# Kernel optimization log

Hardware: AMD Instinct MI355X
Metric: run time of the kernel (lower is better)

## Reference

```python
import jax, jax.numpy as jnp
import numpy as np

B, N, NPOINT, K = 8, 4096, 512, 32
D_IN, D_POS, D_OUT = 64, 64, 128
D = D_IN + D_POS  # 128, channel dim entering Double_SA
EPS = 1e-5


def _gather(pts, idx):
    # pts [B,N,C], idx [B,...] -> [B,...,C]
    return jax.vmap(lambda p, i: p[i])(pts, idx)


def _bn(x, p):
    # eval-mode BatchNorm over last (channel) dim; p = [gamma, beta, mean, var]
    g, b, m, v = p
    return g * (x - m) * jax.lax.rsqrt(v + EPS) + b


def _fps(xyz, start):
    # iterative farthest point sampling, vectorized over batch
    Bb, Nn, _ = xyz.shape
    def step(carry, _):
        dist, far = carry  # dist [B,N], far [B]
        c = jnp.take_along_axis(xyz, far[:, None, None], axis=1)  # [B,1,3]
        d = jnp.sum((xyz - c) ** 2, -1)
        dist = jnp.minimum(dist, d)
        return (dist, jnp.argmax(dist, -1)), far
    init = (jnp.full((Bb, Nn), 1e10, xyz.dtype), start)
    _, idx = jax.lax.scan(step, init, None, length=NPOINT)
    return idx.T  # [B, NPOINT]


def _forward(xyz, points, fps_start, pos_w1, pos_b1, pos_bn1, pos_w2, pos_b2, pos_bn2,
             nsa_wq, nsa_bq, nsa_wk, nsa_bk, nsa_wv, nsa_bv, nsa_gamma, gam_gamma,
             cat_w1, cat_b1, cat_bn1, cat_w2, cat_b2, cat_bn2, sc_w, sc_b, sc_bn):
    fps_idx = _fps(xyz, fps_start)                 # [B,S]
    center_xyz = _gather(xyz, fps_idx)             # [B,S,3]
    # brute-force KNN: squared distances center -> all points, take k smallest
    d2 = (jnp.sum(center_xyz ** 2, -1)[:, :, None] + jnp.sum(xyz ** 2, -1)[:, None, :]
          - 2.0 * jnp.einsum('bsc,bnc->bsn', center_xyz, xyz))  # [B,S,N]
    neg_d, knn_idx = jax.lax.top_k(-d2, K)
    knn_dist = -neg_d                               # [B,S,K], ascending
    grouped_xyz = _gather(xyz, knn_idx)             # [B,S,K,3]
    grouped_pts = _gather(points, knn_idx)          # [B,S,K,D_IN]
    # PosEmbeding: cat(center, neighbor, relative, dist) -> MLP(10 -> Dpos/2 -> Dpos)
    center = jnp.broadcast_to(center_xyz[:, :, None, :], grouped_xyz.shape)
    feat = jnp.concatenate([center, grouped_xyz, grouped_xyz - center, knn_dist[..., None]], -1)
    h = jax.nn.relu(_bn(feat @ pos_w1 + pos_b1, pos_bn1))
    pos = jax.nn.relu(_bn(h @ pos_w2 + pos_b2, pos_bn2))
    x = jnp.concatenate([pos, grouped_pts], -1)     # [B,S,K,D]
    # Neighbor_SA_New: per-group self-attention over K neighbors
    q = x @ nsa_wq + nsa_bq                         # [B,S,K,D//8]
    k = x @ nsa_wk + nsa_bk
    v = x @ nsa_wv + nsa_bv                         # [B,S,K,D]
    attn = jax.nn.softmax(jnp.einsum('bskc,bsjc->bskj', q, k), axis=-1)
    nei = nsa_gamma * jnp.einsum('bskj,bsjd->bskd', attn, v) + x
    # GAM: attention between groups over flattened K*D features
    flat = x.reshape(B, NPOINT, K * D)
    ga = jax.nn.softmax(jnp.einsum('bsd,btd->bst', flat, flat), axis=-1)  # [B,S,S]
    grp = gam_gamma * jnp.einsum('bst,btd->bsd', ga, flat).reshape(B, NPOINT, K, D) + x
    dsa = jnp.concatenate([nei, grp], -1)           # [B,S,K,2D]
    main = _bn(jax.nn.relu(_bn(dsa @ cat_w1 + cat_b1, cat_bn1)) @ cat_w2 + cat_b2, cat_bn2)
    sc = jax.nn.relu(_bn(grouped_pts @ sc_w + sc_b, sc_bn))
    new_points = jnp.max(jax.nn.relu(main + sc), axis=2)  # [B,S,D_OUT]
    return center_xyz, new_points


def setup_inputs():
    ks = jax.random.split(jax.random.key(0), 40)
    def w(i, shape, s=0.05):
        return s * jax.random.normal(ks[i], shape, jnp.float32)
    def bnp(i, c):
        k1, k2, k3, k4 = jax.random.split(ks[i], 4)
        return jnp.stack([jax.random.uniform(k1, (c,), jnp.float32, 0.5, 1.5),
                          0.1 * jax.random.normal(k2, (c,), jnp.float32),
                          0.1 * jax.random.normal(k3, (c,), jnp.float32),
                          jax.random.uniform(k4, (c,), jnp.float32, 0.5, 1.5)])
    return dict(
        xyz=jax.random.normal(ks[0], (B, N, 3), jnp.float32),
        points=jax.random.normal(ks[1], (B, N, D_IN), jnp.float32),
        fps_start=jax.random.randint(ks[2], (B,), 0, N),
        pos_w1=w(3, (10, D_POS // 2)), pos_b1=w(4, (D_POS // 2,)), pos_bn1=bnp(5, D_POS // 2),
        pos_w2=w(6, (D_POS // 2, D_POS)), pos_b2=w(7, (D_POS,)), pos_bn2=bnp(8, D_POS),
        nsa_wq=w(9, (D, D // 8)), nsa_bq=w(10, (D // 8,)),
        nsa_wk=w(11, (D, D // 8)), nsa_bk=w(12, (D // 8,)),
        nsa_wv=w(13, (D, D)), nsa_bv=w(14, (D,)),
        nsa_gamma=jnp.array([0.5], jnp.float32),
        gam_gamma=jnp.array([0.5], jnp.float32),
        cat_w1=w(15, (2 * D, 2 * D)), cat_b1=w(16, (2 * D,)), cat_bn1=bnp(17, 2 * D),
        cat_w2=w(18, (2 * D, D_OUT)), cat_b2=w(19, (D_OUT,)), cat_bn2=bnp(20, D_OUT),
        sc_w=w(21, (D_IN, D_OUT)), sc_b=w(22, (D_OUT,)), sc_bn=bnp(23, D_OUT),
    )


def reference(xyz, points, fps_start, pos_w1, pos_b1, pos_bn1, pos_w2, pos_b2, pos_bn2,
              nsa_wq, nsa_bq, nsa_wk, nsa_bk, nsa_wv, nsa_bv, nsa_gamma, gam_gamma,
              cat_w1, cat_b1, cat_bn1, cat_w2, cat_b2, cat_bn2, sc_w, sc_b, sc_bn):
    return _forward(xyz, points, fps_start, pos_w1, pos_b1, pos_bn1, pos_w2, pos_b2, pos_bn2,
                    nsa_wq, nsa_bq, nsa_wk, nsa_bk, nsa_wv, nsa_bv, nsa_gamma, gam_gamma,
                    cat_w1, cat_b1, cat_bn1, cat_w2, cat_b2, cat_bn2, sc_w, sc_b, sc_bn)
```

## Files before the change

### kernel.cpp

```cpp
#include <hip/hip_runtime.h>
#include <stdint.h>
#include <float.h>

typedef unsigned int uint;

#define NB 8
#define NPTS 4096
#define NS 512
#define NKN 32

__device__ int   g_fps_idx[NB*NS];
__device__ int   g_knn_idx[NB*NS*NKN];
__device__ float g_knn_d2 [NB*NS*NKN];
__device__ float g_posb   [(size_t)NB*NS*NKN*64];
__device__ float g_ga     [(size_t)NB*NS*NS];
__device__ float g_gp     [(size_t)4*NB*NS*NS];
__device__ float g_dsa    [(size_t)NB*NS*NKN*256];

__device__ __forceinline__ unsigned long long shfl_down_u64(unsigned long long v, int off){
  int lo = __shfl_down((int)(unsigned)v, off);
  int hi = __shfl_down((int)(unsigned)(v >> 32), off);
  return ((unsigned long long)(unsigned)hi << 32) | (unsigned)lo;
}
__device__ __forceinline__ unsigned long long u64max(unsigned long long a, unsigned long long b){
  return a > b ? a : b;
}
__device__ __forceinline__ unsigned long long u64min(unsigned long long a, unsigned long long b){
  return a < b ? a : b;
}
__device__ __forceinline__ void ldf8(const float* p, float* d){
  float4 a = *(const float4*)p, b = *(const float4*)(p+4);
  d[0]=a.x; d[1]=a.y; d[2]=a.z; d[3]=a.w; d[4]=b.x; d[5]=b.y; d[6]=b.z; d[7]=b.w;
}
__device__ __forceinline__ int read_start(const int* __restrict__ start, int b){
  int w1 = start[1], w3 = start[3], w5 = start[5], w7 = start[7];
  bool is64 = ((w1 | w3 | w5 | w7) == 0);
  int v = is64 ? start[2*b] : start[b];
  return v & (NPTS - 1);
}

__device__ __forceinline__ void load_flat8(const float* __restrict__ points,
                                           int b, int row, int n, float* d){
  const int k = n >> 7, col = n & 63;
  if (n & 64){
    const int idx = g_knn_idx[((b << 9) + row)*32 + k];
    ldf8(points + (((size_t)b << 12) + idx)*64 + col, d);
  } else {
    ldf8(g_posb + (((size_t)((b << 9) + row))*32 + k)*64 + col, d);
  }
}
__device__ __forceinline__ float4 load_flat4(const float* __restrict__ points,
                                             int b, int row, int n){
  const int k = n >> 7, d = n & 127;
  if (d & 64){
    const int idx = g_knn_idx[((b << 9) + row)*32 + k];
    return *(const float4*)(points + (((size_t)b << 12) + idx)*64 + (d & 63));
  } else {
    return *(const float4*)(g_posb + (((size_t)((b << 9) + row))*32 + k)*64 + d);
  }
}
__device__ __forceinline__ void load_gram8(const float* __restrict__ points,
                                           int b, int row, int kc, float* d){
  if (kc < 2048){
    ldf8(g_posb + ((size_t)((b << 9) + row))*2048 + kc, d);
  } else {
    const int kc2 = kc - 2048, kg = kc2 >> 6, col = kc2 & 63;
    const int idx = g_knn_idx[((b << 9) + row)*32 + kg];
    ldf8(points + (((size_t)b << 12) + idx)*64 + col, d);
  }
}

__global__ __launch_bounds__(256) void k_fps(const float* __restrict__ xyz,
                                             const int* __restrict__ start,
                                             float* __restrict__ center_out){
#pragma clang fp contract(off)
  const int b = blockIdx.x, tid = threadIdx.x;
  const float* X = xyz + (size_t)b * NPTS * 3;
  __shared__ float sx[NPTS], sy[NPTS], sz[NPTS];
  for (int p = tid; p < NPTS; p += 256){
    sx[p] = X[3*p]; sy[p] = X[3*p+1]; sz[p] = X[3*p+2];
  }
  __shared__ int s_start0;
  if (tid == 0) s_start0 = read_start(start, b);
  __syncthreads();
  float px[16], py[16], pz[16], dist[16];
  for (int i = 0; i < 16; i++){
    int p = tid*16 + i;
    px[i] = sx[p]; py[i] = sy[p]; pz[i] = sz[p];
    dist[i] = 1e10f;
  }
  __shared__ unsigned long long s_k[2][4];
  int cur = s_start0;
  for (int t = 0; t < NS; t++){
    if (tid == 0){
      g_fps_idx[b*NS + t] = cur;
      center_out[(size_t)(b*NS + t)*3 + 0] = sx[cur];
      center_out[(size_t)(b*NS + t)*3 + 1] = sy[cur];
      center_out[(size_t)(b*NS + t)*3 + 2] = sz[cur];
    }
    const float cx = sx[cur], cy = sy[cur], cz = sz[cur];
    float bv = -1.0f; int bi = 0;
#pragma unroll
    for (int i = 0; i < 16; i++){
      float dx = px[i]-cx, dy = py[i]-cy, dz = pz[i]-cz;
      float d = ((dx*dx) + (dy*dy)) + (dz*dz);
      dist[i] = fminf(dist[i], d);
      if (dist[i] > bv){ bv = dist[i]; bi = i; }
    }
    unsigned long long bk = ((unsigned long long)__float_as_uint(bv) << 32)
                          | (unsigned)(NPTS-1 - (tid*16 + bi));
    { unsigned long long a = shfl_down_u64(bk,16), c = shfl_down_u64(bk,32), d = shfl_down_u64(bk,48);
      bk = u64max(u64max(bk,a), u64max(c,d)); }
    { unsigned long long a = shfl_down_u64(bk,4),  c = shfl_down_u64(bk,8),  d = shfl_down_u64(bk,12);
      bk = u64max(u64max(bk,a), u64max(c,d)); }
    { unsigned long long a = shfl_down_u64(bk,1),  c = shfl_down_u64(bk,2),  d = shfl_down_u64(bk,3);
      bk = u64max(u64max(bk,a), u64max(c,d)); }
    const int par = t & 1;
    if ((tid & 63) == 0) s_k[par][tid>>6] = bk;
    __syncthreads();
    unsigned long long m = u64max(u64max(s_k[par][0], s_k[par][1]),
                                  u64max(s_k[par][2], s_k[par][3]));
    cur = NPTS-1 - (int)(unsigned)m;
  }
}

__global__ __launch_bounds__(256) void k_knn(const float* __restrict__ xyz){
#pragma clang fp contract(off)
  const int g = blockIdx.x;
  const int b = g >> 9;
  const int tid = threadIdx.x;
  const float* X = xyz + (size_t)b * NPTS * 3;
  const int cidx = g_fps_idx[g];
  const float cx = X[3*cidx], cy = X[3*cidx+1], cz = X[3*cidx+2];
  const float cs = ((cx*cx) + (cy*cy)) + (cz*cz);
  unsigned long long kl[16];
#pragma unroll
  for (int i = 0; i < 16; i++){
    int p = tid*16 + i;
    float x = X[3*p], y = X[3*p+1], z = X[3*p+2];
    float xs2 = ((x*x) + (y*y)) + (z*z);
    float dt  = ((cx*x) + (cy*y)) + (cz*z);
    float d   = (cs + xs2) - 2.0f*dt;
    unsigned bits = __float_as_uint(d);
    unsigned mono = (bits & 0x80000000u) ? ~bits : (bits ^ 0x80000000u);
    kl[i] = ((unsigned long long)mono << 32) | (unsigned)p;
  }
  __shared__ unsigned long long s_w[2][4];
  unsigned long long last = 0;
  for (int sel = 0; sel < NKN; sel++){
    unsigned long long mk[16];
#pragma unroll
    for (int i = 0; i < 16; i++)
      mk[i] = (kl[i] > last) ? kl[i] : 0xFFFFFFFFFFFFFFFFULL;
#pragma unroll
    for (int st = 8; st; st >>= 1)
      for (int i = 0; i < st; i++) mk[i] = u64min(mk[i], mk[i+st]);
    unsigned long long bk = mk[0];
    { unsigned long long a = shfl_down_u64(bk,16), c = shfl_down_u64(bk,32), d = shfl_down_u64(bk,48);
      bk = u64min(u64min(bk,a), u64min(c,d)); }
    { unsigned long long a = shfl_down_u64(bk,4),  c = shfl_down_u64(bk,8),  d = shfl_down_u64(bk,12);
      bk = u64min(u64min(bk,a), u64min(c,d)); }
    { unsigned long long a = shfl_down_u64(bk,1),  c = shfl_down_u64(bk,2),  d = shfl_down_u64(bk,3);
      bk = u64min(u64min(bk,a), u64min(c,d)); }
    const int par = sel & 1;
    if ((tid & 63) == 0) s_w[par][tid>>6] = bk;
    __syncthreads();
    unsigned long long m = u64min(u64min(s_w[par][0], s_w[par][1]),
                                  u64min(s_w[par][2], s_w[par][3]));
    last = m;
    if (tid == 0){
      unsigned hm = (unsigned)(m >> 32);
      unsigned bits = (hm & 0x80000000u) ? (hm ^ 0x80000000u) : ~hm;
      g_knn_idx[g*NKN + sel] = (int)(unsigned)m;
      g_knn_d2 [g*NKN + sel] = __uint_as_float(bits);
    }
  }
}

__global__ __launch_bounds__(256) void k_posembed(
    const float* __restrict__ xyz,
    const float* __restrict__ w1, const float* __restrict__ b1, const float* __restrict__ bn1,
    const float* __restrict__ w2, const float* __restrict__ b2, const float* __restrict__ bn2){
  __shared__ float w1s[320], a1s[32], d1s[32], w2s[2048], a2s[64], d2s[64];
  const int t = threadIdx.x;
  for (int i = t; i < 320; i += 256) w1s[i] = w1[i];
  for (int i = t; i < 2048; i += 256) w2s[i] = w2[i];
  if (t < 32){
    float g = bn1[t], be = bn1[32+t], m = bn1[64+t], v = bn1[96+t];
    float a = g * rsqrtf(v + 1e-5f);
    a1s[t] = a; d1s[t] = b1[t]*a + (be - m*a);
  }
  if (t < 64){
    float g = bn2[t], be = bn2[64+t], m = bn2[128+t], v = bn2[192+t];
    float a = g * rsqrtf(v + 1e-5f);
    a2s[t] = a; d2s[t] = b2[t]*a + (be - m*a);
  }
  __syncthreads();
  const int row = blockIdx.x*256 + t;
  const int b = row >> 14;
  const int g = row >> 5;
  const float* X = xyz + (size_t)b * NPTS * 3;
  const int ci = g_fps_idx[g];
  const int ni = g_knn_idx[row];
  float c0 = X[3*ci], c1 = X[3*ci+1], c2 = X[3*ci+2];
  float n0 = X[3*ni], n1 = X[3*ni+1], n2 = X[3*ni+2];
  float feat[10] = {c0,c1,c2, n0,n1,n2, n0-c0,n1-c1,n2-c2, g_knn_d2[row]};
  float h[32];
  for (int o = 0; o < 32; o++){
    float acc = 0.f;
    for (int j = 0; j < 10; j++) acc += feat[j]*w1s[j*32+o];
    h[o] = fmaxf(acc*a1s[o] + d1s[o], 0.f);
  }
  float* xr = g_posb + (size_t)row * 64;
  for (int o = 0; o < 64; o++){
    float acc = 0.f;
    for (int j = 0; j < 32; j++) acc += h[j]*w2s[j*64+o];
    xr[o] = fmaxf(acc*a2s[o] + d2s[o], 0.f);
  }
}

__global__ __launch_bounds__(256) void k_gram(const float* __restrict__ points){
  const int b = blockIdx.y, ch = blockIdx.z;
  int ti = 0, rem = blockIdx.x;
  while (rem >= 8 - ti){ rem -= 8 - ti; ti++; }
  const int tj = ti + rem;
  const int i0 = ti * 64, j0 = tj * 64;
  __shared__ float As[32][68];
  __shared__ float Bs[32][68];
  const int t = threadIdx.x, tx = t & 15, ty = t >> 4;
  float acc[4][4] = {};
  const int kbeg = ch * 1024, kend = kbeg + 1024;
  for (int k0 = kbeg; k0 < kend; k0 += 32){
    {
      int r = t >> 2, kk = (t & 3) * 8;
      float ta[8], tb[8];
      load_gram8(points, b, i0+r, k0+kk, ta);
      load_gram8(points, b, j0+r, k0+kk, tb);
      for (int jj = 0; jj < 8; jj++){
        int k = kk + jj;
        int c = (r + (k & 24)) & 63;
        As[k][c] = ta[jj]; Bs[k][c] = tb[jj];
      }
    }
    __syncthreads();
    for (int kk = 0; kk < 32; kk++){
      const int rot = kk & 24;
      const float4 a4 = *(const float4*)(&As[kk][(ty*4 + rot) & 63]);
      const float4 b4 = *(const float4*)(&Bs[kk][(tx*4 + rot) & 63]);
      const float ar[4] = {a4.x,a4.y,a4.z,a4.w};
      const float br[4] = {b4.x,b4.y,b4.z,b4.w};
      for (int ia = 0; ia < 4; ia++)
        for (int ib = 0; ib < 4; ib++) acc[ia][ib] += ar[ia]*br[ib];
    }
    __syncthreads();
  }
  float* C = g_gp + ((size_t)(ch*NB + b)) * NS * NS;
  for (int ia = 0; ia < 4; ia++){
    float4 o = {acc[ia][0], acc[ia][1], acc[ia][2], acc[ia][3]};
    *(float4*)(C + (size_t)(i0+ty*4+ia)*NS + j0 + tx*4) = o;
  }
  if (ti != tj){
    for (int ib = 0; ib < 4; ib++){
      float4 o = {acc[0][ib], acc[1][ib], acc[2][ib], acc[3][ib]};
      *(float4*)(C + (size_t)(j0+tx*4+ib)*NS + i0 + ty*4) = o;
    }
  }
}

__global__ __launch_bounds__(256) void k_gsm(){
  const size_t N = (size_t)NB * NS * NS;
  const size_t base = (size_t)blockIdx.x * NS;
  const int t = threadIdx.x;
  float v0, v1;
  {
    float a0 = g_gp[base + t],       b0 = g_gp[N + base + t];
    float c0 = g_gp[2*N + base + t], d0 = g_gp[3*N + base + t];
    v0 = ((a0 + b0) + c0) + d0;
    float a1 = g_gp[base + t + 256],       b1 = g_gp[N + base + t + 256];
    float c1 = g_gp[2*N + base + t + 256], d1 = g_gp[3*N + base + t + 256];
    v1 = ((a1 + b1) + c1) + d1;
  }
  __shared__ float sm[4], ssum[4];
  float m = fmaxf(v0, v1);
  for (int off = 32; off; off >>= 1) m = fmaxf(m, __shfl_down(m, off));
  if ((t & 63) == 0) sm[t>>6] = m;
  __syncthreads();
  float mm = fmaxf(fmaxf(sm[0], sm[1]), fmaxf(sm[2], sm[3]));
  float e0 = expf(v0 - mm), e1 = expf(v1 - mm);
  float s = e0 + e1;
  for (int off = 32; off; off >>= 1) s += __shfl_down(s, off);
  if ((t & 63) == 0) ssum[t>>6] = s;
  __syncthreads();
  float inv = 1.0f / (ssum[0]+ssum[1]+ssum[2]+ssum[3]);
  g_ga[base + t] = e0*inv;
  g_ga[base + t + 256] = e1*inv;
}

__global__ __launch_bounds__(256) void k_grp(const float* __restrict__ points,
                                             const float* __restrict__ gam_g){
  const int b = blockIdx.y;
  const int s0 = (blockIdx.x >> 6) * 64, n0 = (blockIdx.x & 63) * 64;
  const float* G = g_ga + (size_t)b * NS * NS;
  __shared__ float As[32][68];
  __shared__ float Bs[32][68];
  const int t = threadIdx.x, tx = t & 15, ty = t >> 4;
  float acc[4][4] = {};
  for (int k0 = 0; k0 < NS; k0 += 32){
    {
      int r = t >> 2, kk = (t & 3) * 8;
      const float* pa = G + (size_t)(s0+r)*NS + k0 + kk;
      float4 v0 = *(const float4*)pa, v1 = *(const float4*)(pa+4);
      const float va[8] = {v0.x,v0.y,v0.z,v0.w,v1.x,v1.y,v1.z,v1.w};
      for (int jj = 0; jj < 8; jj++){
        int k = kk + jj;
        As[k][(r + (k & 24)) & 63] = va[jj];
      }
      int k2 = t >> 3, c = (t & 7) * 8;
      float tb[8];
      load_flat8(points, b, k0+k2, n0+c, tb);
      float4 w0 = {tb[0],tb[1],tb[2],tb[3]}, w1 = {tb[4],tb[5],tb[6],tb[7]};
      *(float4*)(&Bs[k2][c])   = w0;
      *(float4*)(&Bs[k2][c+4]) = w1;
    }
    __syncthreads();
    for (int kk = 0; kk < 32; kk++){
      const float4 a4 = *(const float4*)(&As[kk][(ty*4 + (kk & 24)) & 63]);
      const float4 b4 = *(const float4*)(&Bs[kk][tx*4]);
      const float ar[4] = {a4.x,a4.y,a4.z,a4.w};
      const float br[4] = {b4.x,b4.y,b4.z,b4.w};
      for (int ia = 0; ia < 4; ia++)
        for (int ib = 0; ib < 4; ib++) acc[ia][ib] += ar[ia]*br[ib];
    }
    __syncthreads();
  }
  const float gmg = gam_g[0];
  const int n = n0 + tx*4;
  const int kq = n >> 7, dq = n & 127;
  for (int ia = 0; ia < 4; ia++){
    int s = s0 + ty*4 + ia;
    float4 xv = load_flat4(points, b, s, n);
    float4 o = {gmg*acc[ia][0]+xv.x, gmg*acc[ia][1]+xv.y,
                gmg*acc[ia][2]+xv.z, gmg*acc[ia][3]+xv.w};
    *(float4*)(g_dsa + ((size_t)((b*NS + s)*32 + kq))*256 + 128 + dq) = o;
  }
}

__global__ __launch_bounds__(256) void k_nsa(const float* __restrict__ points,
    const float* __restrict__ wq, const float* __restrict__ bq,
    const float* __restrict__ wk, const float* __restrict__ bk,
    const float* __restrict__ wv, const float* __restrict__ bv_,
    const float* __restrict__ nsa_g){
  const int g = blockIdx.y*512 + blockIdx.x;
  const int t = threadIdx.x, b = g >> 9;
  const int r = t >> 3, c = t & 7;
  __shared__ float xs[32][132];
  __shared__ float vs[32][132];
  __shared__ float qs[32][17], ks[32][17];
  __shared__ float at[32][33];
  __shared__ float wqs[2048];
  __shared__ float wks[2048];
  __shared__ float wvs[4096];
  {
    float tmp[8];
    ldf8(g_posb + ((size_t)g*32 + r)*64 + c*8, tmp);
    for (int j = 0; j < 8; j++) xs[r][c*8+j] = tmp[j];
    int idx = g_knn_idx[g*32 + r];
    ldf8(points + ((size_t)b*NPTS + idx)*64 + c*8, tmp);
    for (int j = 0; j < 8; j++) xs[r][64+c*8+j] = tmp[j];
  }
  for (int i = t; i < 512; i += 256){
    ((float4*)wqs)[i] = ((const float4*)wq)[i];
    ((float4*)wks)[i] = ((const float4*)wk)[i];
  }
  __syncthreads();
  {
    float aq0 = bq[c], aq1 = bq[c+8], ak0 = bk[c], ak1 = bk[c+8];
#pragma unroll 8
    for (int j = 0; j < 128; j++){
      float xv = xs[r][j];
      aq0 += xv * wqs[j*16+c];
      aq1 += xv * wqs[j*16+c+8];
      ak0 += xv * wks[j*16+c];
      ak1 += xv * wks[j*16+c+8];
    }
    qs[r][c] = aq0; qs[r][c+8] = aq1; ks[r][c] = ak0; ks[r][c+8] = ak1;
  }
  {
    const float4* bv4 = (const float4*)bv_;
    float4 va = bv4[c], vb = bv4[8+c], vc4 = bv4[16+c], vd = bv4[24+c];
#pragma unroll 1
    for (int t4 = 0; t4 < 4; t4++){
      if (t4) __syncthreads();
      for (int i = t; i < 1024; i += 256)
        ((float4*)wvs)[i] = ((const float4*)wv)[(size_t)t4*1024 + i];
      __syncthreads();
#pragma unroll 4
      for (int jl = 0; jl < 32; jl++){
        float xv = xs[r][t4*32 + jl];
        const float4* row = (const float4*)(wvs + jl*128);
        float4 w0 = row[c], w1 = row[8+c], w2 = row[16+c], w3 = row[24+c];
        va.x += xv*w0.x;  va.y += xv*w0.y;  va.z += xv*w0.z;  va.w += xv*w0.w;
        vb.x += xv*w1.x;  vb.y += xv*w1.y;  vb.z += xv*w1.z;  vb.w += xv*w1.w;
        vc4.x += xv*w2.x; vc4.y += xv*w2.y; vc4.z += xv*w2.z; vc4.w += xv*w2.w;
        vd.x += xv*w3.x;  vd.y += xv*w3.y;  vd.z += xv*w3.z;  vd.w += xv*w3.w;
      }
    }
    float4* vrow = (float4*)(&vs[r][0]);
    vrow[c] = va; vrow[8+c] = vb; vrow[16+c] = vc4; vrow[24+c] = vd;
  }
  __syncthreads();
  float p0, p1, p2, p3;
  {
    float s[4];
    for (int jj = 0; jj < 4; jj++){
      int j = 4*c + jj; float acc = 0.f;
      for (int cc = 0; cc < 16; cc++) acc += qs[r][cc] * ks[j][cc];
      s[jj] = acc;
    }
    float m = fmaxf(fmaxf(s[0], s[1]), fmaxf(s[2], s[3]));
    m = fmaxf(m, __shfl_xor(m, 1));
    m = fmaxf(m, __shfl_xor(m, 2));
    m = fmaxf(m, __shfl_xor(m, 4));
    float e0 = expf(s[0]-m), e1 = expf(s[1]-m), e2 = expf(s[2]-m), e3 = expf(s[3]-m);
    float sum = ((e0 + e1) + (e2 + e3));
    sum += __shfl_xor(sum, 1);
    sum += __shfl_xor(sum, 2);
    sum += __shfl_xor(sum, 4);
    float inv = 1.0f / sum;
    p0 = e0*inv; p1 = e1*inv; p2 = e2*inv; p3 = e3*inv;
    at[r][4*c+0] = p0; at[r][4*c+1] = p1; at[r][4*c+2] = p2; at[r][4*c+3] = p3;
  }
  {
    float4 a0 = {0,0,0,0}, a1 = {0,0,0,0}, a2 = {0,0,0,0}, a3 = {0,0,0,0};
    for (int j = 0; j < 32; j++){
      float a = at[r][j];
      const float4* vrow = (const float4*)(&vs[j][0]);
      float4 w0 = vrow[c], w1 = vrow[8+c], w2 = vrow[16+c], w3 = vrow[24+c];
      a0.x += a*w0.x; a0.y += a*w0.y; a0.z += a*w0.z; a0.w += a*w0.w;
      a1.x += a*w1.x; a1.y += a*w1.y; a1.z += a*w1.z; a1.w += a*w1.w;
      a2.x += a*w2.x; a2.y += a*w2.y; a2.z += a*w2.z; a2.w += a*w2.w;
      a3.x += a*w3.x; a3.y += a*w3.y; a3.z += a*w3.z; a3.w += a*w3.w;
    }
    const float gmn = nsa_g[0];
    float* dst = g_dsa + ((size_t)g*32 + r)*256;
    float4 x0 = *(const float4*)(&xs[r][ 0+4*c]);
    float4 x1 = *(const float4*)(&xs[r][32+4*c]);
    float4 x2 = *(const float4*)(&xs[r][64+4*c]);
    float4 x3 = *(const float4*)(&xs[r][96+4*c]);
    float4 o0 = {gmn*a0.x+x0.x, gmn*a0.y+x0.y, gmn*a0.z+x0.z, gmn*a0.w+x0.w};
    float4 o1 = {gmn*a1.x+x1.x, gmn*a1.y+x1.y, gmn*a1.z+x1.z, gmn*a1.w+x1.w};
    float4 o2 = {gmn*a2.x+x2.x, gmn*a2.y+x2.y, gmn*a2.z+x2.z, gmn*a2.w+x2.w};
    float4 o3 = {gmn*a3.x+x3.x, gmn*a3.y+x3.y, gmn*a3.z+x3.z, gmn*a3.w+x3.w};
    *(float4*)(dst +  0 + 4*c) = o0;
    *(float4*)(dst + 32 + 4*c) = o1;
    *(float4*)(dst + 64 + 4*c) = o2;
    *(float4*)(dst + 96 + 4*c) = o3;
  }
}

__global__ __launch_bounds__(256) void k_mlp(const float* __restrict__ points,
    const float* __restrict__ w1, const float* __restrict__ b1, const float* __restrict__ bn1,
    const float* __restrict__ w2, const float* __restrict__ b2, const float* __restrict__ bn2,
    const float* __restrict__ wsc, const float* __restrict__ bsc, const float* __restrict__ bnsc,
    float* __restrict__ out){
  const int g = blockIdx.y*512 + blockIdx.x;
  const int t = threadIdx.x, b = g >> 9;
  __shared__ float ds[32][260];
  __shared__ float hs[32][260];
  __shared__ float ps[32][68];
  __shared__ float a1s[256], d1s[256];
  __shared__ float red[256];
  for (int i = t; i < 2048; i += 256){
    int r = i >> 6, c = (i & 63) * 4;
    *(float4*)(&ds[r][c]) = *(const float4*)(g_dsa + ((size_t)g*32 + r)*256 + c);
  }
  for (int i = t; i < 512; i += 256){
    int r = i >> 4, c = (i & 15) * 4;
    int idx = g_knn_idx[g*32 + r];
    *(float4*)(&ps[r][c]) = *(const float4*)(points + ((size_t)b*NPTS + idx)*64 + c);
  }
  {
    float gg2 = bn1[t], be = bn1[256+t], m = bn1[512+t], v = bn1[768+t];
    float a = gg2 * rsqrtf(v + 1e-5f);
    a1s[t] = a; d1s[t] = b1[t]*a + (be - m*a);
  }
  __syncthreads();
  {
    const int kg = t >> 6, c0 = (t & 63) * 4;
    float acc[8][4] = {};
    for (int j = 0; j < 256; j += 4){
      float wvv[4][4];
      for (int jj = 0; jj < 4; jj++){
        float4 wrow = *(const float4*)(w1 + (j+jj)*256 + c0);
        wvv[jj][0] = wrow.x; wvv[jj][1] = wrow.y; wvv[jj][2] = wrow.z; wvv[jj][3] = wrow.w;
      }
      for (int r = 0; r < 8; r++){
        const float4 d4 = *(const float4*)(&ds[kg*8+r][j]);
        const float dr[4] = {d4.x, d4.y, d4.z, d4.w};
        for (int jj = 0; jj < 4; jj++)
          for (int i = 0; i < 4; i++) acc[r][i] += dr[jj]*wvv[jj][i];
      }
    }
    for (int r = 0; r < 8; r++){
      float4 o;
      o.x = fmaxf(acc[r][0]*a1s[c0+0] + d1s[c0+0], 0.f);
      o.y = fmaxf(acc[r][1]*a1s[c0+1] + d1s[c0+1], 0.f);
      o.z = fmaxf(acc[r][2]*a1s[c0+2] + d1s[c0+2], 0.f);
      o.w = fmaxf(acc[r][3]*a1s[c0+3] + d1s[c0+3], 0.f);
      *(float4*)(&hs[kg*8+r][c0]) = o;
    }
  }
  __syncthreads();
  {
    const int c = t & 127, kh = t >> 7;
    float g2 = bn2[c], be2 = bn2[128+c], m2 = bn2[256+c], v2 = bn2[384+c];
    float a2 = g2 * rsqrtf(v2 + 1e-5f);
    float d2v = b2[c]*a2 + (be2 - m2*a2);
    float gsc = bnsc[c], besc = bnsc[128+c], msc = bnsc[256+c], vsc = bnsc[384+c];
    float asc = gsc * rsqrtf(vsc + 1e-5f);
    float dscv = bsc[c]*asc + (besc - msc*asc);
    float accm[16] = {};
    for (int j = 0; j < 256; j += 4){
      float w0 = w2[j*128+c], w1v = w2[(j+1)*128+c];
      float w2v = w2[(j+2)*128+c], w3 = w2[(j+3)*128+c];
      for (int r = 0; r < 16; r++){
        const float4 h4 = *(const float4*)(&hs[kh*16+r][j]);
        accm[r] += h4.x*w0; accm[r] += h4.y*w1v; accm[r] += h4.z*w2v; accm[r] += h4.w*w3;
      }
    }
    float accs[16] = {};
    for (int j = 0; j < 64; j += 4){
      float w0 = wsc[j*128+c], w1v = wsc[(j+1)*128+c];
      float w2v = wsc[(j+2)*128+c], w3 = wsc[(j+3)*128+c];
      for (int r = 0; r < 16; r++){
        const float4 p4 = *(const float4*)(&ps[kh*16+r][j]);
        accs[r] += p4.x*w0; accs[r] += p4.y*w1v; accs[r] += p4.z*w2v; accs[r] += p4.w*w3;
      }
    }
    float mx = -1e30f;
    for (int r = 0; r < 16; r++){
      float mainv = accm[r]*a2 + d2v;
      float scv = fmaxf(accs[r]*asc + dscv, 0.f);
      mx = fmaxf(mx, fmaxf(mainv + scv, 0.f));
    }
    red[t] = mx;
  }
  __syncthreads();
  if (t < 128){
    float m = fmaxf(red[t], red[t+128]);
    out[12288 + (size_t)g*128 + t] = m;
  }
}

extern "C" void kernel_launch(void* const* d_in, const int* in_sizes, int n_in,
                              void* d_out, int out_size, void* d_ws, size_t ws_size,
                              hipStream_t stream){
  (void)in_sizes; (void)n_in; (void)d_ws; (void)ws_size; (void)out_size;
  const float* xyz      = (const float*)d_in[0];
  const float* points   = (const float*)d_in[1];
  const int*   fstart   = (const int*)  d_in[2];
  const float* pos_w1   = (const float*)d_in[3];
  const float* pos_b1   = (const float*)d_in[4];
  const float* pos_bn1  = (const float*)d_in[5];
  const float* pos_w2   = (const float*)d_in[6];
  const float* pos_b2   = (const float*)d_in[7];
  const float* pos_bn2  = (const float*)d_in[8];
  const float* nsa_wq   = (const float*)d_in[9];
  const float* nsa_bq   = (const float*)d_in[10];
  const float* nsa_wk   = (const float*)d_in[11];
  const float* nsa_bk   = (const float*)d_in[12];
  const float* nsa_wv   = (const float*)d_in[13];
  const float* nsa_bv   = (const float*)d_in[14];
  const float* nsa_g    = (const float*)d_in[15];
  const float* gam_g    = (const float*)d_in[16];
  const float* cat_w1   = (const float*)d_in[17];
  const float* cat_b1   = (const float*)d_in[18];
  const float* cat_bn1  = (const float*)d_in[19];
  const float* cat_w2   = (const float*)d_in[20];
  const float* cat_b2   = (const float*)d_in[21];
  const float* cat_bn2  = (const float*)d_in[22];
  const float* sc_w     = (const float*)d_in[23];
  const float* sc_b     = (const float*)d_in[24];
  const float* sc_bn    = (const float*)d_in[25];
  float* out = (float*)d_out;

  k_fps     <<<NB, 256, 0, stream>>>(xyz, fstart, out);
  k_knn     <<<NB*NS, 256, 0, stream>>>(xyz);
  k_posembed<<<512, 256, 0, stream>>>(xyz, pos_w1, pos_b1, pos_bn1, pos_w2, pos_b2, pos_bn2);
  k_gram    <<<dim3(36, NB, 4), 256, 0, stream>>>(points);
  k_gsm     <<<NB*NS, 256, 0, stream>>>();
  k_grp     <<<dim3(512, NB), 256, 0, stream>>>(points, gam_g);
  k_nsa     <<<dim3(512, NB), 256, 0, stream>>>(points, nsa_wq, nsa_bq, nsa_wk, nsa_bk,
                                                nsa_wv, nsa_bv, nsa_g);
  k_mlp     <<<dim3(512, NB), 256, 0, stream>>>(points, cat_w1, cat_b1, cat_bn1,
                                                cat_w2, cat_b2, cat_bn2,
                                                sc_w, sc_b, sc_bn, out);
}
```

Before: 1.680 ms.

## Fuse position-embedding MLP into KNN kernel and vectorize point loads

Merges the separate position-embedding kernel into the KNN kernel, so the neighbour indices and distances stay in shared memory instead of going through a global buffer and a second launch. The xyz coordinates are now loaded with float4 vector reads, and the per-selection min scan replaces the masked tree reduction with a single conditional loop. Each block now also loads the MLP weights and does the embedding work for its 32 neighbours, split across 8 threads per row with float4 stores. The cost is extra shared memory and register pressure in the KNN kernel, and the weight loads are repeated in all 4096 blocks.

```diff
diff --git a/kernel.cpp b/kernel.cpp
--- a/kernel.cpp
+++ b/kernel.cpp
@@ -11,7 +11,6 @@
 
 __device__ int   g_fps_idx[NB*NS];
 __device__ int   g_knn_idx[NB*NS*NKN];
-__device__ float g_knn_d2 [NB*NS*NKN];
 __device__ float g_posb   [(size_t)NB*NS*NKN*64];
 __device__ float g_ga     [(size_t)NB*NS*NS];
 __device__ float g_gp     [(size_t)4*NB*NS*NS];
@@ -124,20 +123,47 @@
   }
 }
 
-__global__ __launch_bounds__(256) void k_knn(const float* __restrict__ xyz){
+__global__ __launch_bounds__(256) void k_knn(const float* __restrict__ xyz,
+    const float* __restrict__ w1, const float* __restrict__ b1, const float* __restrict__ bn1,
+    const float* __restrict__ w2, const float* __restrict__ b2, const float* __restrict__ bn2){
 #pragma clang fp contract(off)
   const int g = blockIdx.x;
   const int b = g >> 9;
   const int tid = threadIdx.x;
   const float* X = xyz + (size_t)b * NPTS * 3;
+  __shared__ float w1s[320], a1s[32], d1s[32], w2s[2048], a2s[64], d2s[64];
+  __shared__ int   s_ni[32];
+  __shared__ float s_nd[32];
+  __shared__ unsigned long long s_w[2][4];
+  for (int i = tid; i < 320; i += 256) w1s[i] = w1[i];
+  for (int i = tid; i < 2048; i += 256) w2s[i] = w2[i];
+  if (tid < 32){
+    float gg = bn1[tid], be = bn1[32+tid], m = bn1[64+tid], v = bn1[96+tid];
+    float a = gg * rsqrtf(v + 1e-5f);
+    a1s[tid] = a; d1s[tid] = b1[tid]*a + (be - m*a);
+  }
+  if (tid < 64){
+    float gg = bn2[tid], be = bn2[64+tid], m = bn2[128+tid], v = bn2[192+tid];
+    float a = gg * rsqrtf(v + 1e-5f);
+    a2s[tid] = a; d2s[tid] = b2[tid]*a + (be - m*a);
+  }
   const int cidx = g_fps_idx[g];
   const float cx = X[3*cidx], cy = X[3*cidx+1], cz = X[3*cidx+2];
   const float cs = ((cx*cx) + (cy*cy)) + (cz*cz);
+  float xl[48];
+  {
+    const float4* Xp = (const float4*)(X + tid*48);
+#pragma unroll
+    for (int q = 0; q < 12; q++){
+      float4 v = Xp[q];
+      xl[q*4+0]=v.x; xl[q*4+1]=v.y; xl[q*4+2]=v.z; xl[q*4+3]=v.w;
+    }
+  }
   unsigned long long kl[16];
 #pragma unroll
   for (int i = 0; i < 16; i++){
     int p = tid*16 + i;
-    float x = X[3*p], y = X[3*p+1], z = X[3*p+2];
+    float x = xl[3*i], y = xl[3*i+1], z = xl[3*i+2];
     float xs2 = ((x*x) + (y*y)) + (z*z);
     float dt  = ((cx*x) + (cy*y)) + (cz*z);
     float d   = (cs + xs2) - 2.0f*dt;
@@ -145,17 +171,14 @@
     unsigned mono = (bits & 0x80000000u) ? ~bits : (bits ^ 0x80000000u);
     kl[i] = ((unsigned long long)mono << 32) | (unsigned)p;
   }
-  __shared__ unsigned long long s_w[2][4];
   unsigned long long last = 0;
   for (int sel = 0; sel < NKN; sel++){
-    unsigned long long mk[16];
+    unsigned long long bk = 0xFFFFFFFFFFFFFFFFULL;
 #pragma unroll
-    for (int i = 0; i < 16; i++)
-      mk[i] = (kl[i] > last) ? kl[i] : 0xFFFFFFFFFFFFFFFFULL;
-#pragma unroll
-    for (int st = 8; st; st >>= 1)
-      for (int i = 0; i < st; i++) mk[i] = u64min(mk[i], mk[i+st]);
-    unsigned long long bk = mk[0];
+    for (int i = 0; i < 16; i++){
+      unsigned long long k = kl[i];
+      if (k > last && k < bk) bk = k;
+    }
     { unsigned long long a = shfl_down_u64(bk,16), c = shfl_down_u64(bk,32), d = shfl_down_u64(bk,48);
       bk = u64min(u64min(bk,a), u64min(c,d)); }
     { unsigned long long a = shfl_down_u64(bk,4),  c = shfl_down_u64(bk,8),  d = shfl_down_u64(bk,12);
@@ -169,53 +192,39 @@
                                   u64min(s_w[par][2], s_w[par][3]));
     last = m;
     if (tid == 0){
+      int ni = (int)(unsigned)m;
+      g_knn_idx[g*NKN + sel] = ni;
+      s_ni[sel] = ni;
       unsigned hm = (unsigned)(m >> 32);
       unsigned bits = (hm & 0x80000000u) ? (hm ^ 0x80000000u) : ~hm;
-      g_knn_idx[g*NKN + sel] = (int)(unsigned)m;
-      g_knn_d2 [g*NKN + sel] = __uint_as_float(bits);
-    }
-  }
-}
-
-__global__ __launch_bounds__(256) void k_posembed(
-    const float* __restrict__ xyz,
-    const float* __restrict__ w1, const float* __restrict__ b1, const float* __restrict__ bn1,
-    const float* __restrict__ w2, const float* __restrict__ b2, const float* __restrict__ bn2){
-  __shared__ float w1s[320], a1s[32], d1s[32], w2s[2048], a2s[64], d2s[64];
-  const int t = threadIdx.x;
-  for (int i = t; i < 320; i += 256) w1s[i] = w1[i];
-  for (int i = t; i < 2048; i += 256) w2s[i] = w2[i];
-  if (t < 32){
-    float g = bn1[t], be = bn1[32+t], m = bn1[64+t], v = bn1[96+t];
-    float a = g * rsqrtf(v + 1e-5f);
-    a1s[t] = a; d1s[t] = b1[t]*a + (be - m*a);
-  }
-  if (t < 64){
-    float g = bn2[t], be = bn2[64+t], m = bn2[128+t], v = bn2[192+t];
-    float a = g * rsqrtf(v + 1e-5f);
-    a2s[t] = a; d2s[t] = b2[t]*a + (be - m*a);
-  }
-  __syncthreads();
-  const int row = blockIdx.x*256 + t;
-  const int b = row >> 14;
-  const int g = row >> 5;
-  const float* X = xyz + (size_t)b * NPTS * 3;
-  const int ci = g_fps_idx[g];
-  const int ni = g_knn_idx[row];
-  float c0 = X[3*ci], c1 = X[3*ci+1], c2 = X[3*ci+2];
-  float n0 = X[3*ni], n1 = X[3*ni+1], n2 = X[3*ni+2];
-  float feat[10] = {c0,c1,c2, n0,n1,n2, n0-c0,n1-c1,n2-c2, g_knn_d2[row]};
-  float h[32];
-  for (int o = 0; o < 32; o++){
-    float acc = 0.f;
-    for (int j = 0; j < 10; j++) acc += feat[j]*w1s[j*32+o];
-    h[o] = fmaxf(acc*a1s[o] + d1s[o], 0.f);
-  }
-  float* xr = g_posb + (size_t)row * 64;
-  for (int o = 0; o < 64; o++){
-    float acc = 0.f;
-    for (int j = 0; j < 32; j++) acc += h[j]*w2s[j*64+o];
-    xr[o] = fmaxf(acc*a2s[o] + d2s[o], 0.f);
+      s_nd[sel] = __uint_as_float(bits);
+    }
+  }
+  __syncthreads();
+  {
+    const int r = tid >> 3, c8 = (tid & 7) * 8;
+    const int ni = s_ni[r];
+    float n0 = X[3*ni], n1 = X[3*ni+1], n2 = X[3*ni+2];
+    float feat[10] = {cx,cy,cz, n0,n1,n2, n0-cx,n1-cy,n2-cz, s_nd[r]};
+    float h[32];
+    for (int o = 0; o < 32; o++){
+      float acc = 0.f;
+      for (int j = 0; j < 10; j++) acc += feat[j]*w1s[j*32+o];
+      h[o] = fmaxf(acc*a1s[o] + d1s[o], 0.f);
+    }
+    float o8[8];
+#pragma unroll
+    for (int oo = 0; oo < 8; oo++){
+      int o = c8 + oo;
+      float acc = 0.f;
+      for (int j = 0; j < 32; j++) acc += h[j]*w2s[j*64+o];
+      o8[oo] = fmaxf(acc*a2s[o] + d2s[o], 0.f);
+    }
+    float* xr = g_posb + ((size_t)g*32 + r)*64;
+    float4 v0 = {o8[0], o8[1], o8[2], o8[3]};
+    float4 v1 = {o8[4], o8[5], o8[6], o8[7]};
+    *(float4*)(xr + c8)     = v0;
+    *(float4*)(xr + c8 + 4) = v1;
   }
 }
 
@@ -585,8 +594,7 @@
   float* out = (float*)d_out;
 
   k_fps     <<<NB, 256, 0, stream>>>(xyz, fstart, out);
-  k_knn     <<<NB*NS, 256, 0, stream>>>(xyz);
-  k_posembed<<<512, 256, 0, stream>>>(xyz, pos_w1, pos_b1, pos_bn1, pos_w2, pos_b2, pos_bn2);
+  k_knn     <<<NB*NS, 256, 0, stream>>>(xyz, pos_w1, pos_b1, pos_bn1, pos_w2, pos_b2, pos_bn2);
   k_gram    <<<dim3(36, NB, 4), 256, 0, stream>>>(points);
   k_gsm     <<<NB*NS, 256, 0, stream>>>();
   k_grp     <<<dim3(512, NB), 256, 0, stream>>>(points, gam_g);
```

After: 1.636 ms, median of 2. -2.6%, faster.
